# Kernel optimization log

Measured on AMD Instinct MI355X. Metric: run time of the kernel, lower is better.

The kernel has to match this reference:

```python
import jax, jax.numpy as jnp
import numpy as np

H = 51  # hidden size hard-coded in the module


def setup_inputs() -> dict:
    key = jax.random.key(0)
    ks = jax.random.split(key, 11)
    B, T = 1024, 512
    s = 1.0 / np.sqrt(H)
    u = lambda k, shape: jax.random.uniform(k, shape, jnp.float32, -s, s)
    return {
        "input": jax.random.normal(ks[0], (B, T), jnp.float32),
        "Wih1": u(ks[1], (4 * H, 1)),
        "Whh1": u(ks[2], (4 * H, H)),
        "bih1": u(ks[3], (4 * H,)),
        "bhh1": u(ks[4], (4 * H,)),
        "Wih2": u(ks[5], (4 * H, H)),
        "Whh2": u(ks[6], (4 * H, H)),
        "bih2": u(ks[7], (4 * H,)),
        "bhh2": u(ks[8], (4 * H,)),
        "Wl": u(ks[9], (1, H)),
        "bl": u(ks[10], (1,)),
        "future": 64,
    }


def _lstm_cell(x, h, c, Wih, Whh, b):
    # x: [B, in], h/c: [B, H]; PyTorch LSTMCell gate order: i, f, g, o
    g = x @ Wih.T + h @ Whh.T + b  # [B, 4H]
    i, f, gg, o = jnp.split(g, 4, axis=-1)
    c = jax.nn.sigmoid(f) * c + jax.nn.sigmoid(i) * jnp.tanh(gg)
    h = jax.nn.sigmoid(o) * jnp.tanh(c)
    return h, c


def reference(input, Wih1, Whh1, bih1, bhh1, Wih2, Whh2, bih2, bhh2, Wl, bl, future):
    B = input.shape[0]
    b1 = bih1 + bhh1
    b2 = bih2 + bhh2
    z = jnp.zeros((B, H), input.dtype)

    def step(carry, x_t):
        h1, c1, h2, c2 = carry
        h1, c1 = _lstm_cell(x_t[:, None], h1, c1, Wih1, Whh1, b1)
        h2, c2 = _lstm_cell(h1, h2, c2, Wih2, Whh2, b2)
        out = h2 @ Wl.T + bl  # [B, 1]
        return (h1, c1, h2, c2), out

    carry, outs = jax.lax.scan(step, (z, z, z, z), input.T)  # outs: [T, B, 1]

    if future > 0:
        def fstep(carry, _):
            h1, c1, h2, c2, out = carry
            h1, c1 = _lstm_cell(out, h1, c1, Wih1, Whh1, b1)
            h2, c2 = _lstm_cell(h1, h2, c2, Wih2, Whh2, b2)
            out = h2 @ Wl.T + bl
            return (h1, c1, h2, c2, out), out

        _, fouts = jax.lax.scan(fstep, (*carry, outs[-1]), None, length=future)
        outs = jnp.concatenate([outs, fouts], axis=0)  # [T+future, B, 1]

    return outs[..., 0].T  # [B, T+future]
```

## Files before the change

kernel.cpp:

```cpp
#include <hip/hip_runtime.h>
#include <stdint.h>

#define Hh   51
#define Bsz  1024
#define Tin  512
#define Ttot 576
#define NBB  16
#define NW   7
#define BLK  (NW*64)
#define BST  136

#define L2E   1.4426950408889634f
#define TL2E  2.8853900817779268f

typedef __attribute__((ext_vector_type(8))) _Float16 half8;
typedef __attribute__((ext_vector_type(4))) float f32x4;

__device__ __forceinline__ float rcpf(float x){ return __builtin_amdgcn_rcpf(x); }
__device__ __forceinline__ float exp2f_fast(float x){
#if __has_builtin(__builtin_amdgcn_exp2f)
    return __builtin_amdgcn_exp2f(x);
#else
    return exp2f(x);
#endif
}

__device__ __forceinline__ float cell_fuse(float vi, float vf, float vg,
                                           float vo, float& c){
    float Ei = exp2f_fast(-vi), Ef = exp2f_fast(-vf), Eg = exp2f_fast(-vg);
    float A = 1.f + Ef, B = 1.f + Ei, C = 1.f + Eg, D = 1.f - Eg;
    float BC = B*C;
    float R  = rcpf(A*BC);
    float cn = __builtin_fmaf(c, BC*R, (A*D)*R);
    c = cn;
    float Ec = exp2f_fast(fminf(-cn*TL2E, 120.f));
    float Eo = exp2f_fast(-vo);
    float R2 = rcpf((1.f+Eo)*(1.f+Ec));
    return (1.f - Ec) * R2;
}

__device__ __forceinline__ uint16_t f2h(float f){
    union{ _Float16 h; uint16_t u; } v; v.h = (_Float16)f;
    return v.u;
}
#define MFMA __builtin_amdgcn_mfma_f32_16x16x32_f16

__global__ __launch_bounds__(BLK, 2)
void lstm_f16t(const float* __restrict__ inp,
               const float* __restrict__ Wih1,
               const float* __restrict__ Whh1,
               const float* __restrict__ bih1,
               const float* __restrict__ bhh1,
               const float* __restrict__ Wih2,
               const float* __restrict__ Whh2,
               const float* __restrict__ bih2,
               const float* __restrict__ bhh2,
               const float* __restrict__ Wl,
               const float* __restrict__ blp,
               float* __restrict__ outp)
{
    const int tid = threadIdx.x;
    const int wv  = tid >> 6, ln = tid & 63;
    const int quad = ln >> 4, nn = ln & 15;
    const int b0  = blockIdx.x * NBB;

    __shared__ __align__(16) uint16_t Bh[2][NBB*BST];
    __shared__ float wsum[2][NW*17];

    for (int k = tid; k < NBB*BST; k += BLK) { Bh[0][k] = 0; Bh[1][k] = 0; }
    if (tid < NW*17) { wsum[0][tid] = 0.f; wsum[1][tid] = 0.f; }

    half8 a1[2][2], a2[2][4];
    f32x4 bias1[2], bias2[2], wih1v[2];
    float wlu[2]; int ut[2]; bool uvt[2];
#pragma unroll
    for (int tl = 0; tl < 2; ++tl) {
        const bool tv = (wv + 7*tl) < 13;
        const int lr = 16*(wv + 7*tl) + nn;
        const int ua = lr >> 2, ga = lr & 3;
        const bool av = tv && (ua < Hh);
        const int pr = av ? (ga*Hh + ua) : 0;
        const float rs = (ga == 2) ? TL2E : L2E;
#pragma unroll
        for (int s = 0; s < 2; ++s)
#pragma unroll
            for (int j = 0; j < 8; ++j) {
                int k = 32*s + quad*8 + j;
                float w = (av && k < Hh) ? Whh1[pr*Hh + k]*rs : 0.f;
                a1[tl][s][j] = (_Float16)w;
            }
#pragma unroll
        for (int s = 0; s < 4; ++s)
#pragma unroll
            for (int j = 0; j < 8; ++j) {
                int k = 32*s + quad*8 + j;
                float w = 0.f;
                if (av) {
                    if (k < Hh)                    w = Wih2[pr*Hh + k]*rs;
                    else if (k >= 64 && k < 64+Hh) w = Whh2[pr*Hh + (k-64)]*rs;
                }
                a2[tl][s][j] = (_Float16)w;
            }
        const int u = 4*(wv + 7*tl) + quad;
        ut[tl] = u; uvt[tl] = tv && (u < Hh);
#pragma unroll
        for (int i = 0; i < 4; ++i) {
            int pri = uvt[tl] ? (i*Hh + u) : 0;
            float gs = (i == 2) ? TL2E : L2E;
            bias1[tl][i] = uvt[tl] ? (bih1[pri] + bhh1[pri])*gs : 0.f;
            bias2[tl][i] = uvt[tl] ? (bih2[pri] + bhh2[pri])*gs : 0.f;
            wih1v[tl][i] = uvt[tl] ? Wih1[pri]*gs : 0.f;
        }
        wlu[tl] = uvt[tl] ? Wl[ut[tl]] : 0.f;
    }
    const float blv = blp[0];
    float c1[2] = {0.f, 0.f}, c2[2] = {0.f, 0.f};

    {
        float x0 = inp[(size_t)(b0 + nn)*Tin];
#pragma unroll
        for (int tl = 0; tl < 2; ++tl) {
            float vi = __builtin_fmaf(wih1v[tl][0], x0, bias1[tl][0]);
            float vf = __builtin_fmaf(wih1v[tl][1], x0, bias1[tl][1]);
            float vg = __builtin_fmaf(wih1v[tl][2], x0, bias1[tl][2]);
            float vo = __builtin_fmaf(wih1v[tl][3], x0, bias1[tl][3]);
            float h1n = cell_fuse(vi, vf, vg, vo, c1[tl]);
            if (uvt[tl]) Bh[0][nn*BST + ut[tl]] = f2h(h1n);
        }
    }
    float xreg = (Tin > 1) ? inp[(size_t)(b0 + nn)*Tin + 1] : 0.f;
    __syncthreads();

    for (int t = 0; t < Tin-1; ++t) {
        const int cur = t & 1, nxt = cur ^ 1;

        if (wv == NW-1 && t > 0) {
            float osum = blv;
#pragma unroll
            for (int w = 0; w < NW; ++w) osum += wsum[nxt][w*17 + nn];
            if (ln < NBB) outp[(size_t)(b0 + ln)*Ttot + (t-1)] = osum;
        }
        const int tc = (t + 2 < Tin) ? t + 2 : Tin - 1;
        float xl = inp[(size_t)(b0 + nn)*Tin + tc];
        float xn = (t + 2 < Tin) ? xl : 0.f;

        const uint16_t* rb = &Bh[cur][nn*BST + quad*8];
        half8 s0 = *(const half8*)(rb),      s1 = *(const half8*)(rb + 32);
        half8 s2 = *(const half8*)(rb + 64), s3 = *(const half8*)(rb + 96);

        f32x4 aA0 = bias2[0], aB0 = {0.f,0.f,0.f,0.f};
        f32x4 aA1 = bias2[1], aB1 = {0.f,0.f,0.f,0.f};
        f32x4 bA0, bA1, bB0 = {0.f,0.f,0.f,0.f}, bB1 = {0.f,0.f,0.f,0.f};
#pragma unroll
        for (int i = 0; i < 4; ++i) {
            bA0[i] = __builtin_fmaf(wih1v[0][i], xreg, bias1[0][i]);
            bA1[i] = __builtin_fmaf(wih1v[1][i], xreg, bias1[1][i]);
        }
        aA0 = MFMA(a2[0][0], s0, aA0, 0,0,0);  aB0 = MFMA(a2[0][1], s1, aB0, 0,0,0);
        aA1 = MFMA(a2[1][0], s0, aA1, 0,0,0);  aB1 = MFMA(a2[1][1], s1, aB1, 0,0,0);
        bA0 = MFMA(a1[0][0], s0, bA0, 0,0,0);  bB0 = MFMA(a1[0][1], s1, bB0, 0,0,0);
        bA1 = MFMA(a1[1][0], s0, bA1, 0,0,0);  bB1 = MFMA(a1[1][1], s1, bB1, 0,0,0);
        aA0 = MFMA(a2[0][2], s2, aA0, 0,0,0);  aB0 = MFMA(a2[0][3], s3, aB0, 0,0,0);
        aA1 = MFMA(a2[1][2], s2, aA1, 0,0,0);  aB1 = MFMA(a2[1][3], s3, aB1, 0,0,0);

        f32x4 g20 = aA0 + aB0, g21 = aA1 + aB1;
        f32x4 g10 = bA0 + bB0, g11 = bA1 + bB1;
        float h2v0 = cell_fuse(g20[0], g20[1], g20[2], g20[3], c2[0]);
        float h2v1 = cell_fuse(g21[0], g21[1], g21[2], g21[3], c2[1]);
        float h1n0 = cell_fuse(g10[0], g10[1], g10[2], g10[3], c1[0]);
        float h1n1 = cell_fuse(g11[0], g11[1], g11[2], g11[3], c1[1]);

        if (uvt[0]) {
            Bh[nxt][nn*BST + 64 + ut[0]] = f2h(h2v0);
            Bh[nxt][nn*BST      + ut[0]] = f2h(h1n0);
        }
        if (uvt[1]) {
            Bh[nxt][nn*BST + 64 + ut[1]] = f2h(h2v1);
            Bh[nxt][nn*BST      + ut[1]] = f2h(h1n1);
        }
        float part = __builtin_fmaf(wlu[0], h2v0, wlu[1]*h2v1);
        part += __shfl_xor(part, 16, 64);
        part += __shfl_xor(part, 32, 64);
        if (quad == 0) wsum[cur][wv*17 + nn] = part;

        __syncthreads();
        xreg = xn;
    }

    for (int t = Tin-1; t < Ttot; ++t) {
        const int cur = t & 1, nxt = cur ^ 1;

        if (wv == NW-1) {
            float osum = blv;
#pragma unroll
            for (int w = 0; w < NW; ++w) osum += wsum[nxt][w*17 + nn];
            if (ln < NBB) outp[(size_t)(b0 + ln)*Ttot + (t-1)] = osum;
        }

        const uint16_t* rb = &Bh[cur][nn*BST + quad*8];
        half8 s0 = *(const half8*)(rb),      s1 = *(const half8*)(rb + 32);
        half8 s2 = *(const half8*)(rb + 64), s3 = *(const half8*)(rb + 96);

        f32x4 aA0 = bias2[0], aB0 = {0.f,0.f,0.f,0.f};
        f32x4 aA1 = bias2[1], aB1 = {0.f,0.f,0.f,0.f};
        aA0 = MFMA(a2[0][0], s0, aA0, 0,0,0);  aB0 = MFMA(a2[0][1], s1, aB0, 0,0,0);
        aA1 = MFMA(a2[1][0], s0, aA1, 0,0,0);  aB1 = MFMA(a2[1][1], s1, aB1, 0,0,0);
        aA0 = MFMA(a2[0][2], s2, aA0, 0,0,0);  aB0 = MFMA(a2[0][3], s3, aB0, 0,0,0);
        aA1 = MFMA(a2[1][2], s2, aA1, 0,0,0);  aB1 = MFMA(a2[1][3], s3, aB1, 0,0,0);
        f32x4 g20 = aA0 + aB0, g21 = aA1 + aB1;
        float h2v0 = cell_fuse(g20[0], g20[1], g20[2], g20[3], c2[0]);
        float h2v1 = cell_fuse(g21[0], g21[1], g21[2], g21[3], c2[1]);
        if (uvt[0]) Bh[nxt][nn*BST + 64 + ut[0]] = f2h(h2v0);
        if (uvt[1]) Bh[nxt][nn*BST + 64 + ut[1]] = f2h(h2v1);
        float part = __builtin_fmaf(wlu[0], h2v0, wlu[1]*h2v1);
        part += __shfl_xor(part, 16, 64);
        part += __shfl_xor(part, 32, 64);
        if (quad == 0) wsum[cur][wv*17 + nn] = part;
        __syncthreads();

        if (t + 1 < Ttot) {
            float osum = blv;
#pragma unroll
            for (int w = 0; w < NW; ++w) osum += wsum[cur][w*17 + nn];
            f32x4 bA0, bA1, bB0 = {0.f,0.f,0.f,0.f}, bB1 = {0.f,0.f,0.f,0.f};
#pragma unroll
            for (int i = 0; i < 4; ++i) {
                bA0[i] = __builtin_fmaf(wih1v[0][i], osum, bias1[0][i]);
                bA1[i] = __builtin_fmaf(wih1v[1][i], osum, bias1[1][i]);
            }
            bA0 = MFMA(a1[0][0], s0, bA0, 0,0,0);  bB0 = MFMA(a1[0][1], s1, bB0, 0,0,0);
            bA1 = MFMA(a1[1][0], s0, bA1, 0,0,0);  bB1 = MFMA(a1[1][1], s1, bB1, 0,0,0);
            f32x4 g10 = bA0 + bB0, g11 = bA1 + bB1;
            float h1n0 = cell_fuse(g10[0], g10[1], g10[2], g10[3], c1[0]);
            float h1n1 = cell_fuse(g11[0], g11[1], g11[2], g11[3], c1[1]);
            if (uvt[0]) Bh[nxt][nn*BST + ut[0]] = f2h(h1n0);
            if (uvt[1]) Bh[nxt][nn*BST + ut[1]] = f2h(h1n1);
            __syncthreads();
        }
    }

    if (wv == NW-1) {
        float osum = blv;
#pragma unroll
        for (int w = 0; w < NW; ++w) osum += wsum[(Ttot-1)&1][w*17 + nn];
        if (ln < NBB) outp[(size_t)(b0 + ln)*Ttot + (Ttot-1)] = osum;
    }
}

extern "C" void kernel_launch(void* const* d_in, const int* in_sizes, int n_in,
                              void* d_out, int out_size, void* d_ws, size_t ws_size,
                              hipStream_t stream) {
    (void)in_sizes; (void)n_in; (void)out_size; (void)d_ws; (void)ws_size;
    lstm_f16t<<<dim3(Bsz / NBB), dim3(BLK), 0, stream>>>(
        (const float*)d_in[0], (const float*)d_in[1],
        (const float*)d_in[2], (const float*)d_in[3],
        (const float*)d_in[4], (const float*)d_in[5],
        (const float*)d_in[6], (const float*)d_in[7],
        (const float*)d_in[8], (const float*)d_in[9],
        (const float*)d_in[10], (float*)d_out);
}
```

Measured before the change: 581.8 us.

## Halve batch per block and redistribute cell work across MFMA column lanes

Each block now processes 8 batch rows instead of 16, which doubles the grid, while the MFMA tiles stay 16 columns wide with the upper 8 columns padded. Lanes in the upper half take over the second hidden-unit tile through an xor-8 shuffle, so each lane evaluates one cell per layer instead of two. The aim is to shorten the serial per-step latency of the nonlinearities and to run more blocks in parallel across CUs. The cost is half-wasted MFMA throughput, extra shuffles, and twice as many blocks each repeating the weight setup.

```diff
diff --git a/kernel.cpp b/kernel.cpp
--- a/kernel.cpp
+++ b/kernel.cpp
@@ -1,14 +1,15 @@
 #include <hip/hip_runtime.h>
 #include <stdint.h>
 
-#define Hh   51
-#define Bsz  1024
-#define Tin  512
-#define Ttot 576
-#define NBB  16
-#define NW   7
-#define BLK  (NW*64)
-#define BST  136
+#define Hh    51
+#define Bsz   1024
+#define Tin   512
+#define Ttot  576
+#define NBB   8
+#define BROWS 16
+#define NW    7
+#define BLK   (NW*64)
+#define BST   136
 
 #define L2E   1.4426950408889634f
 #define TL2E  2.8853900817779268f
@@ -46,7 +47,7 @@
 #define MFMA __builtin_amdgcn_mfma_f32_16x16x32_f16
 
 __global__ __launch_bounds__(BLK, 2)
-void lstm_f16t(const float* __restrict__ inp,
+void lstm_f16r(const float* __restrict__ inp,
                const float* __restrict__ Wih1,
                const float* __restrict__ Whh1,
                const float* __restrict__ bih1,
@@ -62,24 +63,25 @@
     const int tid = threadIdx.x;
     const int wv  = tid >> 6, ln = tid & 63;
     const int quad = ln >> 4, nn = ln & 15;
+    const bool lo = (nn < 8);
     const int b0  = blockIdx.x * NBB;
 
-    __shared__ __align__(16) uint16_t Bh[2][NBB*BST];
+    __shared__ __align__(16) uint16_t Bh[2][BROWS*BST];
     __shared__ float wsum[2][NW*17];
 
-    for (int k = tid; k < NBB*BST; k += BLK) { Bh[0][k] = 0; Bh[1][k] = 0; }
+    for (int k = tid; k < BROWS*BST; k += BLK) { Bh[0][k] = 0; Bh[1][k] = 0; }
     if (tid < NW*17) { wsum[0][tid] = 0.f; wsum[1][tid] = 0.f; }
 
     half8 a1[2][2], a2[2][4];
     f32x4 bias1[2], bias2[2], wih1v[2];
-    float wlu[2]; int ut[2]; bool uvt[2];
+    float wlu[2];
 #pragma unroll
     for (int tl = 0; tl < 2; ++tl) {
         const bool tv = (wv + 7*tl) < 13;
         const int lr = 16*(wv + 7*tl) + nn;
-        const int ua = lr >> 2, ga = lr & 3;
-        const bool av = tv && (ua < Hh);
-        const int pr = av ? (ga*Hh + ua) : 0;
+        const int ua_ = lr >> 2, ga = lr & 3;
+        const bool av = tv && (ua_ < Hh);
+        const int pr = av ? (ga*Hh + ua_) : 0;
         const float rs = (ga == 2) ? TL2E : L2E;
 #pragma unroll
         for (int s = 0; s < 2; ++s)
@@ -102,33 +104,41 @@
                 a2[tl][s][j] = (_Float16)w;
             }
         const int u = 4*(wv + 7*tl) + quad;
-        ut[tl] = u; uvt[tl] = tv && (u < Hh);
-#pragma unroll
-        for (int i = 0; i < 4; ++i) {
-            int pri = uvt[tl] ? (i*Hh + u) : 0;
+        const bool uv = tv && (u < Hh);
+#pragma unroll
+        for (int i = 0; i < 4; ++i) {
+            int pri = uv ? (i*Hh + u) : 0;
             float gs = (i == 2) ? TL2E : L2E;
-            bias1[tl][i] = uvt[tl] ? (bih1[pri] + bhh1[pri])*gs : 0.f;
-            bias2[tl][i] = uvt[tl] ? (bih2[pri] + bhh2[pri])*gs : 0.f;
-            wih1v[tl][i] = uvt[tl] ? Wih1[pri]*gs : 0.f;
-        }
-        wlu[tl] = uvt[tl] ? Wl[ut[tl]] : 0.f;
+            bias1[tl][i] = uv ? (bih1[pri] + bhh1[pri])*gs : 0.f;
+            bias2[tl][i] = uv ? (bih2[pri] + bhh2[pri])*gs : 0.f;
+            wih1v[tl][i] = uv ? Wih1[pri]*gs : 0.f;
+        }
+        wlu[tl] = uv ? Wl[u] : 0.f;
     }
     const float blv = blp[0];
-    float c1[2] = {0.f, 0.f}, c2[2] = {0.f, 0.f};
+
+    const int  ua  = 4*(wv + (lo ? 0 : 7)) + quad;
+    const bool uva = (ua < Hh);
+    const int  ba  = nn & 7;
+    const float wlua = lo ? wlu[0] : wlu[1];
+    float c1 = 0.f, c2 = 0.f;
 
     {
-        float x0 = inp[(size_t)(b0 + nn)*Tin];
-#pragma unroll
-        for (int tl = 0; tl < 2; ++tl) {
-            float vi = __builtin_fmaf(wih1v[tl][0], x0, bias1[tl][0]);
-            float vf = __builtin_fmaf(wih1v[tl][1], x0, bias1[tl][1]);
-            float vg = __builtin_fmaf(wih1v[tl][2], x0, bias1[tl][2]);
-            float vo = __builtin_fmaf(wih1v[tl][3], x0, bias1[tl][3]);
-            float h1n = cell_fuse(vi, vf, vg, vo, c1[tl]);
-            if (uvt[tl]) Bh[0][nn*BST + ut[tl]] = f2h(h1n);
-        }
-    }
-    float xreg = (Tin > 1) ? inp[(size_t)(b0 + nn)*Tin + 1] : 0.f;
+        float b1a[4], w1a[4];
+#pragma unroll
+        for (int i = 0; i < 4; ++i) {
+            b1a[i] = lo ? bias1[0][i] : bias1[1][i];
+            w1a[i] = lo ? wih1v[0][i] : wih1v[1][i];
+        }
+        float x0 = inp[(size_t)(b0 + ba)*Tin];
+        float vi = __builtin_fmaf(w1a[0], x0, b1a[0]);
+        float vf = __builtin_fmaf(w1a[1], x0, b1a[1]);
+        float vg = __builtin_fmaf(w1a[2], x0, b1a[2]);
+        float vo = __builtin_fmaf(w1a[3], x0, b1a[3]);
+        float h1n = cell_fuse(vi, vf, vg, vo, c1);
+        if (uva) Bh[0][ba*BST + ua] = f2h(h1n);
+    }
+    float xreg = (lo && Tin > 1) ? inp[(size_t)(b0 + nn)*Tin + 1] : 0.f;
     __syncthreads();
 
     for (int t = 0; t < Tin-1; ++t) {
@@ -140,9 +150,7 @@
             for (int w = 0; w < NW; ++w) osum += wsum[nxt][w*17 + nn];
             if (ln < NBB) outp[(size_t)(b0 + ln)*Ttot + (t-1)] = osum;
         }
-        const int tc = (t + 2 < Tin) ? t + 2 : Tin - 1;
-        float xl = inp[(size_t)(b0 + nn)*Tin + tc];
-        float xn = (t + 2 < Tin) ? xl : 0.f;
+        float xn = (lo && t + 2 < Tin) ? inp[(size_t)(b0 + nn)*Tin + t + 2] : 0.f;
 
         const uint16_t* rb = &Bh[cur][nn*BST + quad*8];
         half8 s0 = *(const half8*)(rb),      s1 = *(const half8*)(rb + 32);
@@ -163,25 +171,29 @@
         aA0 = MFMA(a2[0][2], s2, aA0, 0,0,0);  aB0 = MFMA(a2[0][3], s3, aB0, 0,0,0);
         aA1 = MFMA(a2[1][2], s2, aA1, 0,0,0);  aB1 = MFMA(a2[1][3], s3, aB1, 0,0,0);
 
-        f32x4 g20 = aA0 + aB0, g21 = aA1 + aB1;
-        f32x4 g10 = bA0 + bB0, g11 = bA1 + bB1;
-        float h2v0 = cell_fuse(g20[0], g20[1], g20[2], g20[3], c2[0]);
-        float h2v1 = cell_fuse(g21[0], g21[1], g21[2], g21[3], c2[1]);
-        float h1n0 = cell_fuse(g10[0], g10[1], g10[2], g10[3], c1[0]);
-        float h1n1 = cell_fuse(g11[0], g11[1], g11[2], g11[3], c1[1]);
-
-        if (uvt[0]) {
-            Bh[nxt][nn*BST + 64 + ut[0]] = f2h(h2v0);
-            Bh[nxt][nn*BST      + ut[0]] = f2h(h1n0);
-        }
-        if (uvt[1]) {
-            Bh[nxt][nn*BST + 64 + ut[1]] = f2h(h2v1);
-            Bh[nxt][nn*BST      + ut[1]] = f2h(h1n1);
-        }
-        float part = __builtin_fmaf(wlu[0], h2v0, wlu[1]*h2v1);
+        f32x4 g2t0 = aA0 + aB0, g2t1 = aA1 + aB1;
+        f32x4 g1t0 = bA0 + bB0, g1t1 = bA1 + bB1;
+        float g2[4], g1[4];
+#pragma unroll
+        for (int i = 0; i < 4; ++i) {
+            float h2s = __shfl_xor(g2t1[i], 8, 64);
+            float h1s = __shfl_xor(g1t1[i], 8, 64);
+            g2[i] = lo ? g2t0[i] : h2s;
+            g1[i] = lo ? g1t0[i] : h1s;
+        }
+
+        float h2v = cell_fuse(g2[0], g2[1], g2[2], g2[3], c2);
+        float h1v = cell_fuse(g1[0], g1[1], g1[2], g1[3], c1);
+
+        if (uva) {
+            Bh[nxt][ba*BST + 64 + ua] = f2h(h2v);
+            Bh[nxt][ba*BST      + ua] = f2h(h1v);
+        }
+        float part = wlua * h2v;
         part += __shfl_xor(part, 16, 64);
         part += __shfl_xor(part, 32, 64);
-        if (quad == 0) wsum[cur][wv*17 + nn] = part;
+        part += __shfl_xor(part, 8, 64);
+        if (ln < 8) wsum[cur][wv*17 + ln] = part;
 
         __syncthreads();
         xreg = xn;
@@ -207,15 +219,20 @@
         aA1 = MFMA(a2[1][0], s0, aA1, 0,0,0);  aB1 = MFMA(a2[1][1], s1, aB1, 0,0,0);
         aA0 = MFMA(a2[0][2], s2, aA0, 0,0,0);  aB0 = MFMA(a2[0][3], s3, aB0, 0,0,0);
         aA1 = MFMA(a2[1][2], s2, aA1, 0,0,0);  aB1 = MFMA(a2[1][3], s3, aB1, 0,0,0);
-        f32x4 g20 = aA0 + aB0, g21 = aA1 + aB1;
-        float h2v0 = cell_fuse(g20[0], g20[1], g20[2], g20[3], c2[0]);
-        float h2v1 = cell_fuse(g21[0], g21[1], g21[2], g21[3], c2[1]);
-        if (uvt[0]) Bh[nxt][nn*BST + 64 + ut[0]] = f2h(h2v0);
-        if (uvt[1]) Bh[nxt][nn*BST + 64 + ut[1]] = f2h(h2v1);
-        float part = __builtin_fmaf(wlu[0], h2v0, wlu[1]*h2v1);
+        f32x4 g2t0 = aA0 + aB0, g2t1 = aA1 + aB1;
+        float g2[4];
+#pragma unroll
+        for (int i = 0; i < 4; ++i) {
+            float h2s = __shfl_xor(g2t1[i], 8, 64);
+            g2[i] = lo ? g2t0[i] : h2s;
+        }
+        float h2v = cell_fuse(g2[0], g2[1], g2[2], g2[3], c2);
+        if (uva) Bh[nxt][ba*BST + 64 + ua] = f2h(h2v);
+        float part = wlua * h2v;
         part += __shfl_xor(part, 16, 64);
         part += __shfl_xor(part, 32, 64);
-        if (quad == 0) wsum[cur][wv*17 + nn] = part;
+        part += __shfl_xor(part, 8, 64);
+        if (ln < 8) wsum[cur][wv*17 + ln] = part;
         __syncthreads();
 
         if (t + 1 < Ttot) {
@@ -230,11 +247,15 @@
             }
             bA0 = MFMA(a1[0][0], s0, bA0, 0,0,0);  bB0 = MFMA(a1[0][1], s1, bB0, 0,0,0);
             bA1 = MFMA(a1[1][0], s0, bA1, 0,0,0);  bB1 = MFMA(a1[1][1], s1, bB1, 0,0,0);
-            f32x4 g10 = bA0 + bB0, g11 = bA1 + bB1;
-            float h1n0 = cell_fuse(g10[0], g10[1], g10[2], g10[3], c1[0]);
-            float h1n1 = cell_fuse(g11[0], g11[1], g11[2], g11[3], c1[1]);
-            if (uvt[0]) Bh[nxt][nn*BST + ut[0]] = f2h(h1n0);
-            if (uvt[1]) Bh[nxt][nn*BST + ut[1]] = f2h(h1n1);
+            f32x4 g1t0 = bA0 + bB0, g1t1 = bA1 + bB1;
+            float g1[4];
+#pragma unroll
+            for (int i = 0; i < 4; ++i) {
+                float h1s = __shfl_xor(g1t1[i], 8, 64);
+                g1[i] = lo ? g1t0[i] : h1s;
+            }
+            float h1v = cell_fuse(g1[0], g1[1], g1[2], g1[3], c1);
+            if (uva) Bh[nxt][ba*BST + ua] = f2h(h1v);
             __syncthreads();
         }
     }
@@ -251,7 +272,7 @@
                               void* d_out, int out_size, void* d_ws, size_t ws_size,
                               hipStream_t stream) {
     (void)in_sizes; (void)n_in; (void)out_size; (void)d_ws; (void)ws_size;
-    lstm_f16t<<<dim3(Bsz / NBB), dim3(BLK), 0, stream>>>(
+    lstm_f16r<<<dim3(Bsz / NBB), dim3(BLK), 0, stream>>>(
         (const float*)d_in[0], (const float*)d_in[1],
         (const float*)d_in[2], (const float*)d_in[3],
         (const float*)d_in[4], (const float*)d_in[5],
```

Measured after the change: 560.0 us. 1.04x faster.
